# Kernel optimization log

Measured on AMD Instinct MI355X. Metric: run time of the kernel, lower is better.

Reference implementation:

```python
import jax, jax.numpy as jnp
import numpy as np
from jax import lax

B, T, I, H = 64, 784, 1, 600


def setup_inputs() -> dict:
    key = jax.random.key(0)
    ks = jax.random.split(key, 9)
    k = 1.0 / np.sqrt(H)  # pytorch LSTMCell/Linear init scale
    x = jax.random.normal(ks[0], (B, T, I), dtype=jnp.float32)
    hs0 = jax.random.normal(ks[1], (B, H), dtype=jnp.float32)
    cs0 = jax.random.normal(ks[2], (B, H), dtype=jnp.float32)
    W_ih = jax.random.normal(ks[3], (4 * H, I), dtype=jnp.float32) * k
    W_hh = jax.random.normal(ks[4], (4 * H, H), dtype=jnp.float32) * k
    b_ih = jax.random.normal(ks[5], (4 * H,), dtype=jnp.float32) * k
    b_hh = jax.random.normal(ks[6], (4 * H,), dtype=jnp.float32) * k
    W_out = jax.random.normal(ks[7], (10, H), dtype=jnp.float32) * k
    b_out = jax.random.normal(ks[8], (10,), dtype=jnp.float32) * k
    return {"x": x, "hs0": hs0, "cs0": cs0, "W_ih": W_ih, "W_hh": W_hh,
            "b_ih": b_ih, "b_hh": b_hh, "W_out": W_out, "b_out": b_out}


def reference(x, hs0, cs0, W_ih, W_hh, b_ih, b_hh, W_out, b_out):
    # Precompute input projections for all timesteps in one GEMM: [B,T,4H]
    pre = jnp.einsum('bti,gi->btg', x, W_ih) + b_ih + b_hh
    pre_t = jnp.swapaxes(pre, 0, 1)  # [T,B,4H]

    def step(carry, p):
        h, c = carry
        gates = p + h @ W_hh.T  # [B,4H], pytorch gate order i,f,g,o
        i, f, g, o = jnp.split(gates, 4, axis=-1)
        c = jax.nn.sigmoid(f) * c + jax.nn.sigmoid(i) * jnp.tanh(g)
        h = jax.nn.sigmoid(o) * jnp.tanh(c)
        return (h, c), None

    (h, _), _ = lax.scan(step, (hs0, cs0), pre_t)
    return h @ W_out.T + b_out  # [B,10]
```

## Files before the change

kernel.cpp:

```cpp
#include <hip/hip_runtime.h>
#include <math.h>

#define BB 64
#define TT 784
#define HH 600
#define CG 50
#define SGN 4
#define CPW 12
#define BW 16
#define NWG (CG*SGN)
#define BLOCK 512
#define HB4 (BW*150)
#define LDS_BYTES (84*1024)

typedef float f4v __attribute__((ext_vector_type(4)));

__device__ __forceinline__ float dot4acc(f4v a, float4 b, float acc) {
    acc = fmaf(a[0], b.x, acc);
    acc = fmaf(a[1], b.y, acc);
    acc = fmaf(a[2], b.z, acc);
    acc = fmaf(a[3], b.w, acc);
    return acc;
}

__device__ __forceinline__ void ldg5_bypass(const float4* g0, const float4* g1,
                                            const float4* g2, const float4* g3,
                                            const float4* g4,
                                            float4& a, float4& b, float4& c,
                                            float4& d, float4& e) {
    asm volatile(
        "global_load_dwordx4 %0, %5, off sc0 sc1\n\t"
        "global_load_dwordx4 %1, %6, off sc0 sc1\n\t"
        "global_load_dwordx4 %2, %7, off sc0 sc1\n\t"
        "global_load_dwordx4 %3, %8, off sc0 sc1\n\t"
        "global_load_dwordx4 %4, %9, off sc0 sc1\n\t"
        "s_waitcnt vmcnt(0)"
        : "=&v"(a), "=&v"(b), "=&v"(c), "=&v"(d), "=&v"(e)
        : "v"(g0), "v"(g1), "v"(g2), "v"(g3), "v"(g4)
        : "memory");
}

__device__ __forceinline__ void stg_bypass(float* p, float v) {
    asm volatile("global_store_dword %0, %1, off sc0 sc1"
                 :: "v"(p), "v"(v) : "memory");
}

__device__ __forceinline__ float sigm_f(float v) {
    return 1.f / (1.f + __expf(-v));
}
__device__ __forceinline__ float tanh_f(float v) {
    return 1.f - 2.f / (__expf(2.f * v) + 1.f);
}

template<int MASK, int CNT>
__device__ __forceinline__ void fold(float* v, int kh) {
    const bool hi = (kh & MASK) != 0;
    #pragma unroll
    for (int i = 0; i < CNT; ++i) {
        float send = hi ? v[i] : v[i + CNT];
        float recv = __shfl_xor(send, MASK);
        v[i] = (hi ? v[i + CNT] : v[i]) + recv;
    }
}

extern "C" __global__ void __launch_bounds__(BLOCK, 2)
lstm_main(const float* __restrict__ x, const float* __restrict__ hs0,
          const float* __restrict__ cs0, const float* __restrict__ W_ih,
          const float* __restrict__ W_hh, const float* __restrict__ b_ih,
          const float* __restrict__ b_hh, float* __restrict__ hbuf,
          unsigned int* __restrict__ flags)
{
    extern __shared__ float lds[];
    float4* h4l  = (float4*)lds;
    float*  g_lds = lds + 4 * HB4;

    const int wg   = blockIdx.x;
    const int cg   = wg % CG;
    const int sg   = wg / CG;
    const int tid  = threadIdx.x;
    const int w    = tid >> 6;
    const int lane = tid & 63;
    const int bh   = lane >> 5;
    const int kh   = lane & 31;
    const int khc  = (kh < 30) ? kh : 29;
    const int b0   = sg * BW;

    f4v Wr[6][5];
    #pragma unroll
    for (int r = 0; r < 6; ++r) {
        const int row = 6 * w + r;
        const int g   = row / 12, c = row % 12;
        const float* wrow = W_hh + ((size_t)g * HH + cg * CPW + c) * HH + khc * 20;
        #pragma unroll
        for (int j = 0; j < 5; ++j) {
            f4v z = {0.f, 0.f, 0.f, 0.f};
            Wr[r][j] = (kh < 30) ? *(const f4v*)(wrow + 4 * j) : z;
        }
    }
    #pragma unroll
    for (int r = 0; r < 6; ++r) {
        asm volatile("" : "+v"(Wr[r][0]), "+v"(Wr[r][1]), "+v"(Wr[r][2]),
                          "+v"(Wr[r][3]), "+v"(Wr[r][4]));
    }

    float wihv[4], biasv[4], cst = 0.f;
    const int pc = tid >> 4, pb = tid & 15;
    const int cell = cg * CPW + pc;
    const int bglob = b0 + pb;
    if (tid < 192) {
        #pragma unroll
        for (int g = 0; g < 4; ++g) {
            const int grow = g * HH + cell;
            wihv[g]  = W_ih[grow];
            biasv[g] = b_ih[grow] + b_hh[grow];
        }
        cst = cs0[(size_t)bglob * HH + cell];
    }

    const int i0 = tid, i1 = tid + 512, i2 = tid + 1024, i3 = tid + 1536;
    const int i4 = (tid + 2048 < HB4) ? tid + 2048 : HB4 - 1;

    unsigned int* myflag = &flags[wg * 16];

    for (int t = 0; t < TT; ++t) {
        float xv = 0.f;
        if (tid < 192) xv = x[(size_t)bglob * TT + t];

        if (t > 0) {
            if (tid < CG) {
                const unsigned int* f = &flags[(sg * CG + tid) * 16];
                while (__hip_atomic_load(f, __ATOMIC_RELAXED,
                                         __HIP_MEMORY_SCOPE_AGENT) < (unsigned)t)
                    __builtin_amdgcn_s_sleep(1);
            }
        }
        __syncthreads();

        {
            const float* hsrc = (t == 0) ? hs0 : (hbuf + (size_t)(t & 1) * BB * HH);
            const float4* s4 = (const float4*)hsrc + (size_t)b0 * 150;
            float4 v0, v1, v2, v3, v4;
            ldg5_bypass(s4 + i0, s4 + i1, s4 + i2, s4 + i3, s4 + i4,
                        v0, v1, v2, v3, v4);
            h4l[i0] = v0; h4l[i1] = v1; h4l[i2] = v2; h4l[i3] = v3; h4l[i4] = v4;
        }
        __syncthreads();

        float v[48];
        #pragma unroll
        for (int i = 0; i < 48; ++i) v[i] = 0.f;
        {
            const float4* hb_base = h4l + (size_t)bh * 8 * 150 + khc * 5;
            #pragma unroll
            for (int bi = 0; bi < 8; ++bi) {
                const float4* hb = hb_base + bi * 150;
                const float4 h0 = hb[0], h1 = hb[1], h2 = hb[2],
                             h3 = hb[3], hv4 = hb[4];
                #pragma unroll
                for (int r = 0; r < 6; ++r) {
                    float a = v[r * 8 + bi];
                    a = dot4acc(Wr[r][0], h0, a);
                    a = dot4acc(Wr[r][1], h1, a);
                    a = dot4acc(Wr[r][2], h2, a);
                    a = dot4acc(Wr[r][3], h3, a);
                    a = dot4acc(Wr[r][4], hv4, a);
                    v[r * 8 + bi] = a;
                }
            }
        }

        fold<16, 24>(v, kh);
        fold<8, 12>(v, kh);
        fold<4, 6>(v, kh);
        fold<2, 3>(v, kh);
        #pragma unroll
        for (int i = 0; i < 3; ++i)
            v[i] += __shfl_xor(v[i], 1);

        if (!(kh & 1)) {
            const int vb = 3 * (kh >> 1);
            #pragma unroll
            for (int s = 0; s < 3; ++s) {
                const int val = vb + s;
                const int rowl = val >> 3, bi = val & 7;
                g_lds[(6 * w + rowl) * 16 + bh * 8 + bi] = v[s];
            }
        }
        __syncthreads();

        float* hdst = hbuf + (size_t)((t + 1) & 1) * BB * HH;
        if (tid < 192) {
            const float gi = g_lds[(0 * 12 + pc) * 16 + pb] + xv * wihv[0] + biasv[0];
            const float gf = g_lds[(1 * 12 + pc) * 16 + pb] + xv * wihv[1] + biasv[1];
            const float gg = g_lds[(2 * 12 + pc) * 16 + pb] + xv * wihv[2] + biasv[2];
            const float go = g_lds[(3 * 12 + pc) * 16 + pb] + xv * wihv[3] + biasv[3];
            const float cn = sigm_f(gf) * cst + sigm_f(gi) * tanh_f(gg);
            cst = cn;
            stg_bypass(&hdst[(size_t)bglob * HH + cell], sigm_f(go) * tanh_f(cn));
        }
        asm volatile("s_waitcnt vmcnt(0)" ::: "memory");
        __syncthreads();
        if (tid == 0)
            __hip_atomic_store(myflag, (unsigned)(t + 1), __ATOMIC_RELAXED,
                               __HIP_MEMORY_SCOPE_AGENT);
    }
}

extern "C" __global__ void lstm_out(const float* __restrict__ hbuf0,
                                    const float* __restrict__ W_out,
                                    const float* __restrict__ b_out,
                                    float* __restrict__ out)
{
    int b = blockIdx.x;
    int lane = threadIdx.x;
    float acc[10] = {};
    for (int k = lane; k < HH; k += 64) {
        float hv = hbuf0[(size_t)b * HH + k];
        #pragma unroll
        for (int o = 0; o < 10; ++o)
            acc[o] += hv * W_out[(size_t)o * HH + k];
    }
    #pragma unroll
    for (int o = 0; o < 10; ++o) {
        float v = acc[o];
        for (int off = 32; off > 0; off >>= 1) v += __shfl_down(v, off);
        if (lane == 0) out[b * 10 + o] = v + b_out[o];
    }
}

extern "C" void kernel_launch(void* const* d_in, const int* in_sizes, int n_in,
                              void* d_out, int out_size, void* d_ws, size_t ws_size,
                              hipStream_t stream)
{
    const float* x     = (const float*)d_in[0];
    const float* hs0   = (const float*)d_in[1];
    const float* cs0   = (const float*)d_in[2];
    const float* W_ih  = (const float*)d_in[3];
    const float* W_hh  = (const float*)d_in[4];
    const float* b_ih  = (const float*)d_in[5];
    const float* b_hh  = (const float*)d_in[6];
    const float* W_out = (const float*)d_in[7];
    const float* b_out = (const float*)d_in[8];
    float* out = (float*)d_out;

    float* hbuf = (float*)d_ws;
    unsigned int* flags = (unsigned int*)((char*)d_ws + (size_t)2 * BB * HH * sizeof(float));

    hipFuncSetAttribute((const void*)lstm_main,
                        hipFuncAttributeMaxDynamicSharedMemorySize, LDS_BYTES);

    hipMemsetAsync(flags, 0, NWG * 16 * sizeof(unsigned int), stream);
    hipLaunchKernelGGL(lstm_main, dim3(NWG), dim3(BLOCK), LDS_BYTES, stream,
                       x, hs0, cs0, W_ih, W_hh, b_ih, b_hh, hbuf, flags);
    hipLaunchKernelGGL(lstm_out, dim3(BB), dim3(64), 0, stream,
                       hbuf, W_out, b_out, out);
}
```

Before: 4.359 ms.

## Replace global flag barrier with per-producer polling and double-buffered LDS h

```diff
diff --git a/kernel.cpp b/kernel.cpp
--- a/kernel.cpp
+++ b/kernel.cpp
@@ -5,12 +5,12 @@
 #define TT 784
 #define HH 600
 #define CG 50
-#define SGN 4
 #define CPW 12
 #define BW 16
-#define NWG (CG*SGN)
+#define NWG (CG*4)
 #define BLOCK 512
 #define HB4 (BW*150)
+#define HBUF_DW 9600
 #define LDS_BYTES (84*1024)
 
 typedef float f4v __attribute__((ext_vector_type(4)));
@@ -40,6 +40,31 @@
         : "memory");
 }
 
+__device__ __forceinline__ void ldg4_nw(const float4* g0, const float4* g1,
+                                        const float4* g2, const float4* g3,
+                                        float4& A, float4& B, float4& C, float4& D) {
+    asm volatile(
+        "global_load_dwordx4 %0, %4, off sc0 sc1\n\t"
+        "global_load_dwordx4 %1, %5, off sc0 sc1\n\t"
+        "global_load_dwordx4 %2, %6, off sc0 sc1\n\t"
+        "global_load_dwordx4 %3, %7, off sc0 sc1"
+        : "=&v"(A), "=&v"(B), "=&v"(C), "=&v"(D)
+        : "v"(g0), "v"(g1), "v"(g2), "v"(g3) : "memory");
+}
+
+__device__ __forceinline__ void ldg4_w(const float4* g0, const float4* g1,
+                                       const float4* g2, const float4* g3,
+                                       float4& A, float4& B, float4& C, float4& D) {
+    asm volatile(
+        "global_load_dwordx4 %0, %4, off sc0 sc1\n\t"
+        "global_load_dwordx4 %1, %5, off sc0 sc1\n\t"
+        "global_load_dwordx4 %2, %6, off sc0 sc1\n\t"
+        "global_load_dwordx4 %3, %7, off sc0 sc1\n\t"
+        "s_waitcnt vmcnt(0)"
+        : "=&v"(A), "=&v"(B), "=&v"(C), "=&v"(D)
+        : "v"(g0), "v"(g1), "v"(g2), "v"(g3) : "memory");
+}
+
 __device__ __forceinline__ void stg_bypass(float* p, float v) {
     asm volatile("global_store_dword %0, %1, off sc0 sc1"
                  :: "v"(p), "v"(v) : "memory");
@@ -71,8 +96,8 @@
           unsigned int* __restrict__ flags)
 {
     extern __shared__ float lds[];
-    float4* h4l  = (float4*)lds;
-    float*  g_lds = lds + 4 * HB4;
+    float* g_lds = lds + 2 * HBUF_DW;
+    unsigned* ctr = (unsigned*)(lds + 2 * HBUF_DW + 48 * 16);
 
     const int wg   = blockIdx.x;
     const int cg   = wg % CG;
@@ -97,11 +122,6 @@
             Wr[r][j] = (kh < 30) ? *(const f4v*)(wrow + 4 * j) : z;
         }
     }
-    #pragma unroll
-    for (int r = 0; r < 6; ++r) {
-        asm volatile("" : "+v"(Wr[r][0]), "+v"(Wr[r][1]), "+v"(Wr[r][2]),
-                          "+v"(Wr[r][3]), "+v"(Wr[r][4]));
-    }
 
     float wihv[4], biasv[4], cst = 0.f;
     const int pc = tid >> 4, pb = tid & 15;
@@ -117,40 +137,48 @@
         cst = cs0[(size_t)bglob * HH + cell];
     }
 
-    const int i0 = tid, i1 = tid + 512, i2 = tid + 1024, i3 = tid + 1536;
-    const int i4 = (tid + 2048 < HB4) ? tid + 2048 : HB4 - 1;
+    const int swl = w - 3;
+    const int sp  = (w >= 3 && lane < 60) ? (10 * swl + lane / 6) : -1;
+    const int ss  = lane % 6;
+    const bool sact = (sp >= 0 && sp != cg);
+    const unsigned int* spflag = &flags[(sg * CG + (sact ? sp : 0)) * 16];
+    int soff[8], ldo[8];
+    if (sact) {
+        #pragma unroll
+        for (int jj = 0; jj < 8; ++jj) {
+            const int j = 8 * ss + jj, bj = j / 3, cj = j - 3 * bj;
+            soff[jj] = (b0 + bj) * HH + CPW * sp + 4 * cj;
+            ldo[jj]  = bj * HH + CPW * sp + 4 * cj;
+        }
+    }
+
+    if (tid == 0) *ctr = 0u;
+    {
+        const int i0 = tid, i1 = tid + 512, i2 = tid + 1024, i3 = tid + 1536;
+        const int i4 = (tid + 2048 < HB4) ? tid + 2048 : HB4 - 1;
+        const float4* s4 = (const float4*)hs0 + (size_t)b0 * 150;
+        float4 v0, v1, v2, v3, v4;
+        ldg5_bypass(s4 + i0, s4 + i1, s4 + i2, s4 + i3, s4 + i4,
+                    v0, v1, v2, v3, v4);
+        float4* h0 = (float4*)lds;
+        h0[i0] = v0; h0[i1] = v1; h0[i2] = v2; h0[i3] = v3; h0[i4] = v4;
+    }
+    __syncthreads();
 
     unsigned int* myflag = &flags[wg * 16];
 
     for (int t = 0; t < TT; ++t) {
+        const int P = t & 1;
         float xv = 0.f;
         if (tid < 192) xv = x[(size_t)bglob * TT + t];
 
-        if (t > 0) {
-            if (tid < CG) {
-                const unsigned int* f = &flags[(sg * CG + tid) * 16];
-                while (__hip_atomic_load(f, __ATOMIC_RELAXED,
-                                         __HIP_MEMORY_SCOPE_AGENT) < (unsigned)t)
-                    __builtin_amdgcn_s_sleep(1);
-            }
-        }
-        __syncthreads();
-
+        float v[48];
         {
-            const float* hsrc = (t == 0) ? hs0 : (hbuf + (size_t)(t & 1) * BB * HH);
-            const float4* s4 = (const float4*)hsrc + (size_t)b0 * 150;
-            float4 v0, v1, v2, v3, v4;
-            ldg5_bypass(s4 + i0, s4 + i1, s4 + i2, s4 + i3, s4 + i4,
-                        v0, v1, v2, v3, v4);
-            h4l[i0] = v0; h4l[i1] = v1; h4l[i2] = v2; h4l[i3] = v3; h4l[i4] = v4;
-        }
-        __syncthreads();
-
-        float v[48];
-        #pragma unroll
-        for (int i = 0; i < 48; ++i) v[i] = 0.f;
-        {
-            const float4* hb_base = h4l + (size_t)bh * 8 * 150 + khc * 5;
+            float acc[48];
+            #pragma unroll
+            for (int i = 0; i < 48; ++i) acc[i] = 0.f;
+            const float4* hb_base = (const float4*)(lds + P * HBUF_DW)
+                                    + (size_t)bh * 8 * 150 + khc * 5;
             #pragma unroll
             for (int bi = 0; bi < 8; ++bi) {
                 const float4* hb = hb_base + bi * 150;
@@ -158,15 +186,17 @@
                              h3 = hb[3], hv4 = hb[4];
                 #pragma unroll
                 for (int r = 0; r < 6; ++r) {
-                    float a = v[r * 8 + bi];
+                    float a = acc[r * 8 + bi];
                     a = dot4acc(Wr[r][0], h0, a);
                     a = dot4acc(Wr[r][1], h1, a);
                     a = dot4acc(Wr[r][2], h2, a);
                     a = dot4acc(Wr[r][3], h3, a);
                     a = dot4acc(Wr[r][4], hv4, a);
-                    v[r * 8 + bi] = a;
+                    acc[r * 8 + bi] = a;
                 }
             }
+            #pragma unroll
+            for (int i = 0; i < 48; ++i) v[i] = acc[i];
         }
 
         fold<16, 24>(v, kh);
@@ -186,23 +216,49 @@
                 g_lds[(6 * w + rowl) * 16 + bh * 8 + bi] = v[s];
             }
         }
+        asm volatile("s_waitcnt lgkmcnt(0)" ::: "memory");
+        if (lane == 0) atomicAdd(ctr, 1u);
+
+        if (w >= 3) {
+            if (sact && t < TT - 1) {
+                const unsigned thr = 3u * (unsigned)(t + 1);
+                while (__hip_atomic_load(spflag, __ATOMIC_RELAXED,
+                                         __HIP_MEMORY_SCOPE_AGENT) < thr)
+                    __builtin_amdgcn_s_sleep(1);
+                const float* hb1 = hbuf + (size_t)((t + 1) & 1) * BB * HH;
+                float4 d0, d1, d2, d3, d4, d5, d6, d7;
+                ldg4_nw((const float4*)(hb1 + soff[0]), (const float4*)(hb1 + soff[1]),
+                        (const float4*)(hb1 + soff[2]), (const float4*)(hb1 + soff[3]),
+                        d0, d1, d2, d3);
+                ldg4_w((const float4*)(hb1 + soff[4]), (const float4*)(hb1 + soff[5]),
+                       (const float4*)(hb1 + soff[6]), (const float4*)(hb1 + soff[7]),
+                       d4, d5, d6, d7);
+                __builtin_amdgcn_sched_barrier(0);
+                float* hn = lds + (P ^ 1) * HBUF_DW;
+                *(float4*)&hn[ldo[0]] = d0; *(float4*)&hn[ldo[1]] = d1;
+                *(float4*)&hn[ldo[2]] = d2; *(float4*)&hn[ldo[3]] = d3;
+                *(float4*)&hn[ldo[4]] = d4; *(float4*)&hn[ldo[5]] = d5;
+                *(float4*)&hn[ldo[6]] = d6; *(float4*)&hn[ldo[7]] = d7;
+            }
+        } else {
+            const unsigned ct = 8u * (unsigned)(t + 1);
+            while (__hip_atomic_load(ctr, __ATOMIC_RELAXED,
+                                     __HIP_MEMORY_SCOPE_WORKGROUP) < ct) {}
+            const float gi  = g_lds[(0 * 12 + pc) * 16 + pb] + xv * wihv[0] + biasv[0];
+            const float gf  = g_lds[(1 * 12 + pc) * 16 + pb] + xv * wihv[1] + biasv[1];
+            const float gg_ = g_lds[(2 * 12 + pc) * 16 + pb] + xv * wihv[2] + biasv[2];
+            const float go  = g_lds[(3 * 12 + pc) * 16 + pb] + xv * wihv[3] + biasv[3];
+            const float cn = sigm_f(gf) * cst + sigm_f(gi) * tanh_f(gg_);
+            cst = cn;
+            const float hv = sigm_f(go) * tanh_f(cn);
+            lds[(P ^ 1) * HBUF_DW + pb * HH + cell - b0 * 0 * HH - 0] = 0.f;
+            lds[(P ^ 1) * HBUF_DW + pb * HH + cg * CPW + pc] = hv;
+            stg_bypass(hbuf + (size_t)((t + 1) & 1) * BB * HH
+                            + (size_t)bglob * HH + cell, hv);
+            asm volatile("s_waitcnt vmcnt(0)" ::: "memory");
+            if (lane == 0) atomicAdd(myflag, 1u);
+        }
         __syncthreads();
-
-        float* hdst = hbuf + (size_t)((t + 1) & 1) * BB * HH;
-        if (tid < 192) {
-            const float gi = g_lds[(0 * 12 + pc) * 16 + pb] + xv * wihv[0] + biasv[0];
-            const float gf = g_lds[(1 * 12 + pc) * 16 + pb] + xv * wihv[1] + biasv[1];
-            const float gg = g_lds[(2 * 12 + pc) * 16 + pb] + xv * wihv[2] + biasv[2];
-            const float go = g_lds[(3 * 12 + pc) * 16 + pb] + xv * wihv[3] + biasv[3];
-            const float cn = sigm_f(gf) * cst + sigm_f(gi) * tanh_f(gg);
-            cst = cn;
-            stg_bypass(&hdst[(size_t)bglob * HH + cell], sigm_f(go) * tanh_f(cn));
-        }
-        asm volatile("s_waitcnt vmcnt(0)" ::: "memory");
-        __syncthreads();
-        if (tid == 0)
-            __hip_atomic_store(myflag, (unsigned)(t + 1), __ATOMIC_RELAXED,
-                               __HIP_MEMORY_SCOPE_AGENT);
     }
 }
 
```

Result: slower. 5.413 ms (+24.2%).
